# Kernel optimization log

Hardware: AMD Instinct MI355X
Metric: run time of the kernel (lower is better)

The kernel has to match this reference:

```python
import jax, jax.numpy as jnp
import numpy as np

MAX_EMBED = 1024
MAX_HEADS = 16
MIN_WIDTH_RATIO = 0.25


def setup_inputs() -> dict:
    key = jax.random.key(0)
    ks = jax.random.split(key, 10)
    B, S, E = 4, 1024, MAX_EMBED
    query = jax.random.normal(ks[0], (B, S, E), dtype=jnp.float32)
    attention_mask = jax.random.randint(ks[1], (B, 1, 1, S), 0, 2, dtype=jnp.int32)
    # SlimmableLinear params (max sizes); kaiming-ish scale ~ 1/sqrt(fan_in)
    scale = 1.0 / np.sqrt(E)
    def lin(kw, kb):
        w = jax.random.uniform(kw, (E, E), dtype=jnp.float32, minval=-scale, maxval=scale)
        b = jax.random.uniform(kb, (E,), dtype=jnp.float32, minval=-scale, maxval=scale)
        return w, b
    q_w, q_b = lin(ks[2], ks[3])
    k_w, k_b = lin(ks[4], ks[5])
    v_w, v_b = lin(ks[6], ks[7])
    o_w, o_b = lin(ks[8], ks[9])
    return {"query": query, "attention_mask": attention_mask,
            "q_w": q_w, "q_b": q_b, "k_w": k_w, "k_b": k_b,
            "v_w": v_w, "v_b": v_b, "o_w": o_w, "o_b": o_b,
            "width": 768}


def _slim_linear(x, w, b, width):
    # weight stored [out, in] like torch; slice to [width, width]
    return x[..., :width] @ w[:width, :width].T + b[:width]


def reference(query, attention_mask, q_w, q_b, k_w, k_b, v_w, v_b, o_w, o_b, width):
    min_width = int(MAX_EMBED * MIN_WIDTH_RATIO)
    width = max(min_width, min(int(width), MAX_EMBED))
    num_heads = max(1, width * MAX_HEADS // MAX_EMBED)
    head_dim = width // num_heads
    B, S, _ = query.shape

    q = _slim_linear(query, q_w, q_b, width)  # [B,S,width]
    k = _slim_linear(query, k_w, k_b, width)  # key=query (self-attn)
    v = _slim_linear(query, v_w, v_b, width)

    q = q.reshape(B, S, num_heads, head_dim).transpose(0, 2, 1, 3)  # [B,H,S,D]
    k = k.reshape(B, S, num_heads, head_dim).transpose(0, 2, 1, 3)
    v = v.reshape(B, S, num_heads, head_dim).transpose(0, 2, 1, 3)

    scores = jnp.einsum('bhqd,bhkd->bhqk', q, k) / jnp.sqrt(jnp.float32(head_dim))
    scores = jnp.where(attention_mask == 0, jnp.float32(-1e9), scores)
    attn_weights = jax.nn.softmax(scores, axis=-1)  # [B,H,S,S]
    attn_output = jnp.einsum('bhqk,bhkd->bhqd', attn_weights, v)
    attn_output = attn_output.transpose(0, 2, 1, 3).reshape(B, S, width)
    output = attn_output @ o_w[:width, :width].T + o_b[:width]
    return output, attn_weights
```

## Files before the change

kernel.cpp:

```cpp
#include <hip/hip_runtime.h>

#define Bn 4
#define Sn 1024
#define En 1024
#define Wn 768
#define Hn 12
#define Dn 64
#define XE ((size_t)Bn * Sn * Wn)

typedef __attribute__((ext_vector_type(8))) short short8;
typedef __attribute__((ext_vector_type(4))) short short4v;
typedef __attribute__((ext_vector_type(4))) float floatx4;

#define MFMA16(A, B, C) __builtin_amdgcn_mfma_f32_16x16x32_bf16(A, B, C, 0, 0, 0)

__device__ __forceinline__ unsigned short f2bf_rn(float f) {
    unsigned int u = __float_as_uint(f);
    unsigned int r = u + 0x7fffu + ((u >> 16) & 1u);
    return (unsigned short)(r >> 16);
}
__device__ __forceinline__ float bf2f(unsigned short h) {
    return __uint_as_float(((unsigned int)h) << 16);
}

__device__ __forceinline__ void gload_lds16(const unsigned short* g, unsigned short* l) {
    __builtin_amdgcn_global_load_lds(
        (const __attribute__((address_space(1))) void*)g,
        (__attribute__((address_space(3))) void*)l, 16, 0, 0);
}

__global__ __launch_bounds__(256) void prep_kernel(
    const float* __restrict__ x,
    const float* __restrict__ qw, const float* __restrict__ kw,
    const float* __restrict__ vw, const float* __restrict__ ow,
    const float* __restrict__ qb, const float* __restrict__ kb,
    const float* __restrict__ vb,
    unsigned short* __restrict__ xh, unsigned short* __restrict__ xl,
    unsigned short* __restrict__ wqh, unsigned short* __restrict__ wql,
    unsigned short* __restrict__ woh, unsigned short* __restrict__ wol,
    float* __restrict__ bq)
{
    const int bx = blockIdx.x;
    const float* src; unsigned short *dh, *dl; int e;
    if (bx < 3072) {
        e = (bx * 256 + threadIdx.x) * 4;
        src = x; dh = xh; dl = xl;
    } else if (bx < 3072 + 1728) {
        int bb = bx - 3072; int which = bb / 576;
        e = ((bb - which * 576) * 256 + threadIdx.x) * 4;
        src = (which == 0) ? qw : (which == 1) ? kw : vw;
        dh = wqh + (size_t)which * Wn * Wn;
        dl = wql + (size_t)which * Wn * Wn;
    } else if (bx < 3072 + 1728 + 576) {
        e = ((bx - 3072 - 1728) * 256 + threadIdx.x) * 4;
        src = ow; dh = woh; dl = wol;
    } else {
        int t = (bx - 3072 - 1728 - 576) * 256 + threadIdx.x;
        if (t < Wn) bq[t] = qb[t];
        else if (t < 2 * Wn) bq[t] = kb[t - Wn];
        else if (t < 3 * Wn) bq[t] = vb[t - 2 * Wn];
        return;
    }
    int row = e / Wn, col = e - row * Wn;
    float4 v = *(const float4*)(src + (size_t)row * En + col);
    float f[4] = {v.x, v.y, v.z, v.w};
    short4v h, l;
    #pragma unroll
    for (int i = 0; i < 4; ++i) {
        unsigned short hh = f2bf_rn(f[i]);
        h[i] = (short)hh;
        l[i] = (short)f2bf_rn(f[i] - bf2f(hh));
    }
    *(short4v*)(dh + e) = h;
    *(short4v*)(dl + e) = l;
}

__global__ __launch_bounds__(256) void qkv_mfma_kernel(
    const unsigned short* __restrict__ xh, const unsigned short* __restrict__ xl,
    const unsigned short* __restrict__ wh, const unsigned short* __restrict__ wl,
    const float* __restrict__ bq,
    unsigned short* __restrict__ qh_o, unsigned short* __restrict__ kh_o,
    unsigned short* __restrict__ vt_o)
{
    __shared__ __align__(16) unsigned short Ah[128 * 32];
    __shared__ __align__(16) unsigned short Al[128 * 32];
    __shared__ __align__(16) unsigned short Bh[128 * 32];
    __shared__ __align__(16) unsigned short Bl[128 * 32];

    const int tid = threadIdx.x;
    const int wave = tid >> 6, lane = tid & 63;
    const int quad = lane >> 4, l16 = lane & 15;
    const int m0 = blockIdx.x * 128, n0 = blockIdx.y * 128;
    const int wm = wave >> 1, wn = wave & 1;
    const int which = n0 / Wn;
    const bool full = (which == 2);

    floatx4 acc[4][4] = {};

    const unsigned short* gsrc = (wave == 0) ? xh : (wave == 1) ? xl
                               : (wave == 2) ? wh : wl;
    unsigned short* ldst = (wave == 0) ? Ah : (wave == 1) ? Al
                         : (wave == 2) ? Bh : Bl;
    const int base_row = (wave < 2) ? m0 : n0;
    const int r_in = lane >> 2;
    const int cs = (lane & 3) ^ (r_in & 3);

    for (int k0 = 0; k0 < Wn; k0 += 32) {
        if (full || wave == 0 || wave == 2) {
            #pragma unroll
            for (int i = 0; i < 8; ++i) {
                int r = i * 16 + r_in;
                const unsigned short* gp =
                    gsrc + (size_t)(base_row + r) * Wn + k0 + cs * 8;
                gload_lds16(gp, ldst + i * 512);
            }
        }
        __syncthreads();

        short8 afh[4], afl[4], bfh[4], bfl[4];
        #pragma unroll
        for (int t = 0; t < 4; ++t) {
            int mr = wm * 64 + t * 16 + l16;
            int ca = quad ^ (mr & 3);
            afh[t] = *(const short8*)(Ah + mr * 32 + ca * 8);
            if (full) afl[t] = *(const short8*)(Al + mr * 32 + ca * 8);
            int nr = wn * 64 + t * 16 + l16;
            int cb = quad ^ (nr & 3);
            bfh[t] = *(const short8*)(Bh + nr * 32 + cb * 8);
            if (full) bfl[t] = *(const short8*)(Bl + nr * 32 + cb * 8);
        }
        #pragma unroll
        for (int mt = 0; mt < 4; ++mt)
            #pragma unroll
            for (int nt = 0; nt < 4; ++nt) {
                acc[mt][nt] = MFMA16(afh[mt], bfh[nt], acc[mt][nt]);
                if (full) {
                    acc[mt][nt] = MFMA16(afh[mt], bfl[nt], acc[mt][nt]);
                    acc[mt][nt] = MFMA16(afl[mt], bfh[nt], acc[mt][nt]);
                }
            }
        __syncthreads();
    }

    const int b = m0 >> 10;
    #pragma unroll
    for (int nt = 0; nt < 4; ++nt) {
        const int ng = n0 + wn * 64 + nt * 16 + l16;
        const float bias = bq[ng];
        const int f = ng - which * Wn;
        const int h = f >> 6, d = f & 63;
        #pragma unroll
        for (int mt = 0; mt < 4; ++mt) {
            const int mbase = m0 + wm * 64 + mt * 16 + quad * 4;
            const int s0 = mbase & (Sn - 1);
            if (which < 2) {
                unsigned short* oq = which ? kh_o : qh_o;
                size_t idx = (((size_t)(b * Hn + h)) * Sn + s0) * Dn + d;
                #pragma unroll
                for (int r = 0; r < 4; ++r)
                    oq[idx + (size_t)r * Dn] = f2bf_rn(acc[mt][nt][r] + bias);
            } else {
                size_t idx = (((size_t)(b * Hn + h)) * Dn + d) * Sn + s0;
                short4v pk;
                #pragma unroll
                for (int r = 0; r < 4; ++r)
                    pk[r] = (short)f2bf_rn(acc[mt][nt][r] + bias);
                *(short4v*)(vt_o + idx) = pk;
            }
        }
    }
}

__global__ __launch_bounds__(512) void attn_fused_kernel(
    const unsigned short* __restrict__ qh, const unsigned short* __restrict__ kh,
    const unsigned short* __restrict__ vt, const int* __restrict__ mask,
    float* __restrict__ attn,
    unsigned short* __restrict__ aoh, unsigned short* __restrict__ aol)
{
    __shared__ __align__(16) unsigned short Ps[8][16 * 72];
    __shared__ float msk[Sn];
    __shared__ float Lsum[8][16];
    __shared__ __align__(16) float Obuf[4][16][68];

    const int tid = threadIdx.x;
    const int wave = tid >> 6, lane = tid & 63;
    const int quad = lane >> 4, l16 = lane & 15;
    const int pair = wave >> 1, hf = wave & 1;
    const int qt = blockIdx.x;
    const int h = blockIdx.y, b = blockIdx.z;
    const int bh = b * Hn + h;
    const size_t kvb = (size_t)bh * Sn * Dn;
    const size_t vbase = (size_t)bh * Dn * Sn;

    if (tid < 256) {
        int4 mi = *(const int4*)(mask + b * Sn + tid * 4);
        msk[tid * 4 + 0] = (float)mi.x;
        msk[tid * 4 + 1] = (float)mi.y;
        msk[tid * 4 + 2] = (float)mi.z;
        msk[tid * 4 + 3] = (float)mi.w;
    }

    const int qrow = qt * 64 + pair * 16 + l16;
    short8 qf[2];
    {
        const unsigned short* qp = qh + kvb + (size_t)qrow * Dn + quad * 8;
        qf[0] = *(const short8*)(qp);
        qf[1] = *(const short8*)(qp + 32);
    }
    __syncthreads();

    short8 Pr[16];
    float lsumr[4] = {0.f, 0.f, 0.f, 0.f};
    const int kbase = hf * 512;

    #pragma unroll
    for (int kk = 0; kk < 8; ++kk) {
        const int k0 = kbase + kk * 64;
        #pragma unroll
        for (int ct = 0; ct < 4; ++ct) {
            const int key = k0 + ct * 16 + l16;
            const unsigned short* kp = kh + kvb + (size_t)key * Dn + quad * 8;
            short8 kf0 = *(const short8*)(kp);
            short8 kf1 = *(const short8*)(kp + 32);
            floatx4 acc = {0.f, 0.f, 0.f, 0.f};
            acc = MFMA16(qf[0], kf0, acc);
            acc = MFMA16(qf[1], kf1, acc);
            const float mv = msk[key];
            #pragma unroll
            for (int r = 0; r < 4; ++r) {
                const float e = __expf(acc[r] * 0.125f) * mv;
                lsumr[r] += e;
                Ps[wave][(quad * 4 + r) * 72 + ct * 16 + l16] = f2bf_rn(e);
            }
        }
        Pr[kk * 2 + 0] = *(const short8*)&Ps[wave][l16 * 72 + quad * 8];
        Pr[kk * 2 + 1] = *(const short8*)&Ps[wave][l16 * 72 + 32 + quad * 8];
    }

    #pragma unroll
    for (int r = 0; r < 4; ++r) {
        float v = lsumr[r];
        v += __shfl_xor(v, 1, 64);
        v += __shfl_xor(v, 2, 64);
        v += __shfl_xor(v, 4, 64);
        v += __shfl_xor(v, 8, 64);
        lsumr[r] = v;
    }
    if (l16 == 0) {
        #pragma unroll
        for (int r = 0; r < 4; ++r) Lsum[wave][quad * 4 + r] = lsumr[r];
    }
    __syncthreads();

    float li[4];
    #pragma unroll
    for (int r = 0; r < 4; ++r) {
        const float lv = Lsum[pair * 2][quad * 4 + r] + Lsum[pair * 2 + 1][quad * 4 + r];
        li[r] = (lv > 0.f) ? 1.f / lv : 0.f;
    }
    float lt;
    {
        const float lv = Lsum[pair * 2][l16] + Lsum[pair * 2 + 1][l16];
        lt = (lv > 0.f) ? 1.f / lv : 0.f;
    }

    floatx4 oacc[4] = {};
    float* aprow = attn + ((size_t)bh * Sn + qrow) * Sn;

    #pragma unroll
    for (int kk = 0; kk < 8; ++kk) {
        const int k0 = kbase + kk * 64;
        #pragma unroll
        for (int ksp = 0; ksp < 2; ++ksp) {
            const short8 pf = Pr[kk * 2 + ksp];
            float4 f0, f1;
            f0.x = bf2f((unsigned short)pf[0]) * lt;
            f0.y = bf2f((unsigned short)pf[1]) * lt;
            f0.z = bf2f((unsigned short)pf[2]) * lt;
            f0.w = bf2f((unsigned short)pf[3]) * lt;
            f1.x = bf2f((unsigned short)pf[4]) * lt;
            f1.y = bf2f((unsigned short)pf[5]) * lt;
            f1.z = bf2f((unsigned short)pf[6]) * lt;
            f1.w = bf2f((unsigned short)pf[7]) * lt;
            float* ap = aprow + k0 + ksp * 32 + quad * 8;
            *(float4*)(ap)     = f0;
            *(float4*)(ap + 4) = f1;
            #pragma unroll
            for (int dt = 0; dt < 4; ++dt) {
                short8 vf = *(const short8*)(vt + vbase
                              + (size_t)(dt * 16 + l16) * Sn + k0 + ksp * 32 + quad * 8);
                oacc[dt] = MFMA16(pf, vf, oacc[dt]);
            }
        }
    }

    if (hf == 1) {
        #pragma unroll
        for (int dt = 0; dt < 4; ++dt)
            #pragma unroll
            for (int r = 0; r < 4; ++r)
                Obuf[pair][quad * 4 + r][dt * 16 + l16] = oacc[dt][r];
    }
    __syncthreads();
    if (hf == 0) {
        const int row0 = qt * 64 + pair * 16 + quad * 4;
        #pragma unroll
        for (int dt = 0; dt < 4; ++dt)
            #pragma unroll
            for (int r = 0; r < 4; ++r) {
                const float o = (oacc[dt][r] + Obuf[pair][quad * 4 + r][dt * 16 + l16]) * li[r];
                const unsigned short hh = f2bf_rn(o);
                const size_t idx = ((size_t)b * Sn + row0 + r) * Wn + h * Dn + dt * 16 + l16;
                aoh[idx] = hh;
                aol[idx] = f2bf_rn(o - bf2f(hh));
            }
    }
}

__global__ __launch_bounds__(256) void oproj_mfma_kernel(
    const unsigned short* __restrict__ aoh, const unsigned short* __restrict__ aol,
    const unsigned short* __restrict__ wh, const unsigned short* __restrict__ wl,
    const float* __restrict__ ob, float* __restrict__ out)
{
    __shared__ __align__(16) unsigned short Ah[64 * 32];
    __shared__ __align__(16) unsigned short Al[64 * 32];
    __shared__ __align__(16) unsigned short Bh[128 * 32];
    __shared__ __align__(16) unsigned short Bl[128 * 32];

    const int tid = threadIdx.x;
    const int wave = tid >> 6, lane = tid & 63;
    const int quad = lane >> 4, l16 = lane & 15;
    const int m0 = blockIdx.x * 64, n0 = blockIdx.y * 128;
    const int wm = wave >> 1, wn = wave & 1;

    floatx4 acc[2][4] = {};

    const int r_in = lane >> 2;
    const int cs = (lane & 3) ^ (r_in & 3);

    for (int k0 = 0; k0 < Wn; k0 += 32) {
        if (wave == 0) {
            #pragma unroll
            for (int i = 0; i < 4; ++i) {
                gload_lds16(aoh + (size_t)(m0 + i * 16 + r_in) * Wn + k0 + cs * 8,
                            Ah + i * 512);
                gload_lds16(aol + (size_t)(m0 + i * 16 + r_in) * Wn + k0 + cs * 8,
                            Al + i * 512);
            }
        } else if (wave == 1) {
            #pragma unroll
            for (int i = 0; i < 8; ++i)
                gload_lds16(wh + (size_t)(n0 + i * 16 + r_in) * Wn + k0 + cs * 8,
                            Bh + i * 512);
        } else if (wave == 2) {
            #pragma unroll
            for (int i = 0; i < 8; ++i)
                gload_lds16(wl + (size_t)(n0 + i * 16 + r_in) * Wn + k0 + cs * 8,
                            Bl + i * 512);
        }
        __syncthreads();

        short8 afh[2], afl[2], bfh[4], bfl[4];
        #pragma unroll
        for (int t = 0; t < 2; ++t) {
            int mr = wm * 32 + t * 16 + l16;
            int ca = quad ^ (mr & 3);
            afh[t] = *(const short8*)(Ah + mr * 32 + ca * 8);
            afl[t] = *(const short8*)(Al + mr * 32 + ca * 8);
        }
        #pragma unroll
        for (int t = 0; t < 4; ++t) {
            int nr = wn * 64 + t * 16 + l16;
            int cb = quad ^ (nr & 3);
            bfh[t] = *(const short8*)(Bh + nr * 32 + cb * 8);
            bfl[t] = *(const short8*)(Bl + nr * 32 + cb * 8);
        }
        #pragma unroll
        for (int mt = 0; mt < 2; ++mt)
            #pragma unroll
            for (int nt = 0; nt < 4; ++nt) {
                acc[mt][nt] = MFMA16(afh[mt], bfh[nt], acc[mt][nt]);
                acc[mt][nt] = MFMA16(afh[mt], bfl[nt], acc[mt][nt]);
                acc[mt][nt] = MFMA16(afl[mt], bfh[nt], acc[mt][nt]);
            }
        __syncthreads();
    }

    #pragma unroll
    for (int nt = 0; nt < 4; ++nt) {
        const int ng = n0 + wn * 64 + nt * 16 + l16;
        const float bias = ob[ng];
        #pragma unroll
        for (int mt = 0; mt < 2; ++mt) {
            const int m = m0 + wm * 32 + mt * 16 + quad * 4;
            #pragma unroll
            for (int r = 0; r < 4; ++r)
                out[(size_t)(m + r) * Wn + ng] = acc[mt][nt][r] + bias;
        }
    }
}

extern "C" void kernel_launch(void* const* d_in, const int* in_sizes, int n_in,
                              void* d_out, int out_size, void* d_ws, size_t ws_size,
                              hipStream_t stream) {
    const float* x    = (const float*)d_in[0];
    const int*   mask = (const int*)  d_in[1];
    const float* qw = (const float*)d_in[2];
    const float* qb = (const float*)d_in[3];
    const float* kw = (const float*)d_in[4];
    const float* kb = (const float*)d_in[5];
    const float* vw = (const float*)d_in[6];
    const float* vb = (const float*)d_in[7];
    const float* ow = (const float*)d_in[8];
    const float* ob = (const float*)d_in[9];

    float* out  = (float*)d_out;
    float* attn = out + XE;

    char* w = (char*)d_ws;
    unsigned short* xh   = (unsigned short*)w;  w += XE * 2;
    unsigned short* xl   = (unsigned short*)w;  w += XE * 2;
    unsigned short* wqh  = (unsigned short*)w;  w += (size_t)3 * Wn * Wn * 2;
    unsigned short* wql  = (unsigned short*)w;  w += (size_t)3 * Wn * Wn * 2;
    unsigned short* woh  = (unsigned short*)w;  w += (size_t)Wn * Wn * 2;
    unsigned short* wol  = (unsigned short*)w;  w += (size_t)Wn * Wn * 2;
    float*          bq   = (float*)w;           w += (size_t)3 * Wn * 4;
    unsigned short* qh   = (unsigned short*)w;  w += XE * 2;
    unsigned short* kh   = (unsigned short*)w;  w += XE * 2;
    unsigned short* vt_w = (unsigned short*)w;  w += XE * 2;

    prep_kernel<<<5385, 256, 0, stream>>>(x, qw, kw, vw, ow, qb, kb, vb,
                                          xh, xl, wqh, wql, woh, wol, bq);

    qkv_mfma_kernel<<<dim3(32, 18), 256, 0, stream>>>(
        xh, xl, wqh, wql, bq, qh, kh, vt_w);

    attn_fused_kernel<<<dim3(16, Hn, Bn), 512, 0, stream>>>(
        qh, kh, vt_w, mask, attn, xh, xl);

    oproj_mfma_kernel<<<dim3(64, 6), 256, 0, stream>>>(
        xh, xl, woh, wol, ob, out);
}
```

Measured before the change: 408.2 us.

## Split attention keys four ways per 16-row block and reorder QKV tile scheduling

Each attention block now handles 16 query rows, with 4 waves each covering a quarter of the keys, instead of 64 rows with key-halves per wave pair. That gives 4x more, smaller blocks. The P staging buffer and the output-reduction buffer now share one aliased shared-memory region, which cuts LDS per block. The QKV kernel also rotates its blockIdx.y mapping so the full-precision V tiles are scheduled first. The goal is better occupancy and load balance, at the cost of redundant mask loads per block and a 4-way cross-wave reduction.

```diff
diff --git a/kernel.cpp b/kernel.cpp
--- a/kernel.cpp
+++ b/kernel.cpp
@@ -90,7 +90,8 @@
     const int tid = threadIdx.x;
     const int wave = tid >> 6, lane = tid & 63;
     const int quad = lane >> 4, l16 = lane & 15;
-    const int m0 = blockIdx.x * 128, n0 = blockIdx.y * 128;
+    const int yy = ((int)blockIdx.y + 12) % 18;
+    const int m0 = blockIdx.x * 128, n0 = yy * 128;
     const int wm = wave >> 1, wn = wave & 1;
     const int which = n0 / Wn;
     const bool full = (which == 2);
@@ -171,28 +172,30 @@
     }
 }
 
-__global__ __launch_bounds__(512) void attn_fused_kernel(
+__global__ __launch_bounds__(256) void attn_fused_kernel(
     const unsigned short* __restrict__ qh, const unsigned short* __restrict__ kh,
     const unsigned short* __restrict__ vt, const int* __restrict__ mask,
     float* __restrict__ attn,
     unsigned short* __restrict__ aoh, unsigned short* __restrict__ aol)
 {
-    __shared__ __align__(16) unsigned short Ps[8][16 * 72];
+    __shared__ __align__(16) char PsObuf[3 * 16 * 68 * 4];
     __shared__ float msk[Sn];
-    __shared__ float Lsum[8][16];
-    __shared__ __align__(16) float Obuf[4][16][68];
+    __shared__ float Lsum[4][16];
+
+    unsigned short (*Ps)[16 * 72] =
+        (unsigned short (*)[16 * 72])PsObuf;
+    float (*Obuf)[16][68] = (float (*)[16][68])PsObuf;
 
     const int tid = threadIdx.x;
     const int wave = tid >> 6, lane = tid & 63;
     const int quad = lane >> 4, l16 = lane & 15;
-    const int pair = wave >> 1, hf = wave & 1;
     const int qt = blockIdx.x;
     const int h = blockIdx.y, b = blockIdx.z;
     const int bh = b * Hn + h;
     const size_t kvb = (size_t)bh * Sn * Dn;
     const size_t vbase = (size_t)bh * Dn * Sn;
 
-    if (tid < 256) {
+    {
         int4 mi = *(const int4*)(mask + b * Sn + tid * 4);
         msk[tid * 4 + 0] = (float)mi.x;
         msk[tid * 4 + 1] = (float)mi.y;
@@ -200,7 +203,7 @@
         msk[tid * 4 + 3] = (float)mi.w;
     }
 
-    const int qrow = qt * 64 + pair * 16 + l16;
+    const int qrow = qt * 16 + l16;
     short8 qf[2];
     {
         const unsigned short* qp = qh + kvb + (size_t)qrow * Dn + quad * 8;
@@ -209,12 +212,12 @@
     }
     __syncthreads();
 
-    short8 Pr[16];
+    short8 Pr[8];
     float lsumr[4] = {0.f, 0.f, 0.f, 0.f};
-    const int kbase = hf * 512;
-
-    #pragma unroll
-    for (int kk = 0; kk < 8; ++kk) {
+    const int kbase = wave * 256;
+
+    #pragma unroll
+    for (int kk = 0; kk < 4; ++kk) {
         const int k0 = kbase + kk * 64;
         #pragma unroll
         for (int ct = 0; ct < 4; ++ct) {
@@ -255,12 +258,13 @@
     float li[4];
     #pragma unroll
     for (int r = 0; r < 4; ++r) {
-        const float lv = Lsum[pair * 2][quad * 4 + r] + Lsum[pair * 2 + 1][quad * 4 + r];
+        const float lv = Lsum[0][quad * 4 + r] + Lsum[1][quad * 4 + r]
+                       + Lsum[2][quad * 4 + r] + Lsum[3][quad * 4 + r];
         li[r] = (lv > 0.f) ? 1.f / lv : 0.f;
     }
     float lt;
     {
-        const float lv = Lsum[pair * 2][l16] + Lsum[pair * 2 + 1][l16];
+        const float lv = Lsum[0][l16] + Lsum[1][l16] + Lsum[2][l16] + Lsum[3][l16];
         lt = (lv > 0.f) ? 1.f / lv : 0.f;
     }
 
@@ -268,7 +272,7 @@
     float* aprow = attn + ((size_t)bh * Sn + qrow) * Sn;
 
     #pragma unroll
-    for (int kk = 0; kk < 8; ++kk) {
+    for (int kk = 0; kk < 4; ++kk) {
         const int k0 = kbase + kk * 64;
         #pragma unroll
         for (int ksp = 0; ksp < 2; ++ksp) {
@@ -294,21 +298,24 @@
         }
     }
 
-    if (hf == 1) {
+    if (wave != 0) {
         #pragma unroll
         for (int dt = 0; dt < 4; ++dt)
             #pragma unroll
             for (int r = 0; r < 4; ++r)
-                Obuf[pair][quad * 4 + r][dt * 16 + l16] = oacc[dt][r];
+                Obuf[wave - 1][quad * 4 + r][dt * 16 + l16] = oacc[dt][r];
     }
     __syncthreads();
-    if (hf == 0) {
-        const int row0 = qt * 64 + pair * 16 + quad * 4;
+    if (wave == 0) {
+        const int row0 = qt * 16 + quad * 4;
         #pragma unroll
         for (int dt = 0; dt < 4; ++dt)
             #pragma unroll
             for (int r = 0; r < 4; ++r) {
-                const float o = (oacc[dt][r] + Obuf[pair][quad * 4 + r][dt * 16 + l16]) * li[r];
+                const float o = (oacc[dt][r]
+                               + Obuf[0][quad * 4 + r][dt * 16 + l16]
+                               + Obuf[1][quad * 4 + r][dt * 16 + l16]
+                               + Obuf[2][quad * 4 + r][dt * 16 + l16]) * li[r];
                 const unsigned short hh = f2bf_rn(o);
                 const size_t idx = ((size_t)b * Sn + row0 + r) * Wn + h * Dn + dt * 16 + l16;
                 aoh[idx] = hh;
@@ -435,7 +442,7 @@
     qkv_mfma_kernel<<<dim3(32, 18), 256, 0, stream>>>(
         xh, xl, wqh, wql, bq, qh, kh, vt_w);
 
-    attn_fused_kernel<<<dim3(16, Hn, Bn), 512, 0, stream>>>(
+    attn_fused_kernel<<<dim3(64, Hn, Bn), 256, 0, stream>>>(
         qh, kh, vt_w, mask, attn, xh, xl);
 
     oproj_mfma_kernel<<<dim3(64, 6), 256, 0, stream>>>(
```

Result: faster. 390.8 us (-4.3%).
